# Performance work log

Measured on AMD Instinct MI355X. Metric: run time of the kernel, lower is better.

Reference implementation:

```python
import jax, jax.numpy as jnp
import numpy as np

DEPTH = 8
DIM = 512
D_INNER = 2 * DIM          # mamba expand=2
D_STATE = 16
D_CONV = 4
DT_RANK = DIM // 16        # 32
B, H, W = 2, 16, 16
EPS = 1e-5


def setup_inputs() -> dict:
    key = jax.random.key(0)
    ks = jax.random.split(key, 8)
    s = 0.02
    f32 = jnp.float32
    x = jax.random.normal(ks[0], (B, DIM, H, W), f32)
    in_proj_w = (jax.random.normal(ks[1], (DEPTH, 2 * D_INNER, DIM), f32) * s)
    conv_w = (jax.random.normal(ks[2], (DEPTH, D_INNER, D_CONV), f32) * 0.1)
    conv_b = jnp.zeros((DEPTH, D_INNER), f32)
    x_proj_w = (jax.random.normal(ks[3], (DEPTH, DT_RANK + 2 * D_STATE, D_INNER), f32) * s)
    dt_proj_w = (jax.random.normal(ks[4], (DEPTH, D_INNER, DT_RANK), f32) * s)
    dt_proj_b = (jax.random.normal(ks[5], (DEPTH, D_INNER), f32) * 0.1)
    # S4D-real init: A = -exp(A_log), A_log = log(1..d_state)
    A_log = jnp.log(jnp.broadcast_to(
        jnp.arange(1, D_STATE + 1, dtype=f32), (DEPTH, D_INNER, D_STATE)))
    D = jnp.ones((DEPTH, D_INNER), f32)
    out_proj_w = (jax.random.normal(ks[6], (DEPTH, DIM, D_INNER), f32) * s)
    norm_w = jnp.ones((DEPTH, DIM), f32)
    final_norm_w = jnp.ones((DIM,), f32)
    return {"x": x, "in_proj_w": in_proj_w, "conv_w": conv_w, "conv_b": conv_b,
            "x_proj_w": x_proj_w, "dt_proj_w": dt_proj_w, "dt_proj_b": dt_proj_b,
            "A_log": A_log, "D": D, "out_proj_w": out_proj_w,
            "norm_w": norm_w, "final_norm_w": final_norm_w}


def _rmsnorm(x, w):
    # rms_norm_ref: no mean subtraction, weight only (bias is None)
    return x * jax.lax.rsqrt(jnp.mean(x * x, axis=-1, keepdims=True) + EPS) * w


def _mixer(h, Wi, cw, cb, Wx, Wdt, bdt, A_log, Dv, Wo):
    # h: [B, L, DIM]
    xz = jnp.einsum('bld,ed->ble', h, Wi)            # [B,L,2*Di]
    xc, z = jnp.split(xz, 2, axis=-1)
    # causal depthwise conv1d (pad left d_conv-1), then SiLU
    xt = xc.transpose(0, 2, 1)                        # [B,Di,L]
    xt = jax.lax.conv_general_dilated(
        xt, cw[:, None, :], (1,), [(D_CONV - 1, 0)],
        feature_group_count=D_INNER)
    xc = jax.nn.silu((xt + cb[None, :, None]).transpose(0, 2, 1))  # [B,L,Di]
    dbl = jnp.einsum('bld,kd->blk', xc, Wx)           # [B,L,dt_rank+2N]
    dtr = dbl[..., :DT_RANK]
    Bm = dbl[..., DT_RANK:DT_RANK + D_STATE]          # [B,L,N]
    Cm = dbl[..., DT_RANK + D_STATE:]                 # [B,L,N]
    dt = jax.nn.softplus(jnp.einsum('blr,dr->bld', dtr, Wdt) + bdt)  # [B,L,Di]
    A = -jnp.exp(A_log)                               # [Di,N]
    dA = jnp.exp(dt[..., None] * A)                   # [B,L,Di,N]
    dBx = (dt * xc)[..., None] * Bm[:, :, None, :]    # [B,L,Di,N]

    def step(s, inp):
        a, bx, c = inp
        s = a * s + bx                                # [B,Di,N]
        return s, jnp.einsum('bdn,bn->bd', s, c)

    s0 = jnp.zeros((xc.shape[0], D_INNER, D_STATE), xc.dtype)
    _, ys = jax.lax.scan(step, s0, (dA.transpose(1, 0, 2, 3),
                                    dBx.transpose(1, 0, 2, 3),
                                    Cm.transpose(1, 0, 2)))
    y = ys.transpose(1, 0, 2) + Dv * xc               # [B,L,Di]
    y = y * jax.nn.silu(z)
    return jnp.einsum('bld,od->blo', y, Wo)           # [B,L,DIM]


def reference(x, in_proj_w, conv_w, conv_b, x_proj_w, dt_proj_w, dt_proj_b,
              A_log, D, out_proj_w, norm_w, final_norm_w):
    Bz, C, Hh, Ww = x.shape
    h = x.reshape(Bz, C, Hh * Ww).transpose(0, 2, 1)  # [B,L,C]
    residual = None
    for i in range(DEPTH):
        # fused add + RMSNorm (prenorm): residual <- h + residual; hn = norm(residual)
        residual = h if residual is None else h + residual
        hn = _rmsnorm(residual, norm_w[i])
        h = _mixer(hn, in_proj_w[i], conv_w[i], conv_b[i], x_proj_w[i],
                   dt_proj_w[i], dt_proj_b[i], A_log[i], D[i], out_proj_w[i])
    # Original module: with return_index=[depth-1], the returned tensor is the
    # post-loop `residual`; the final mixer output and final norm are dead code.
    out = residual.reshape(Bz, Hh, Ww, C)
    return out.transpose(0, 3, 1, 2)
```

## Files before the change

kernel.cpp:

```cpp
#include <hip/hip_runtime.h>
#include <hip/hip_bf16.h>

typedef __bf16 bf16x8 __attribute__((ext_vector_type(8)));
typedef float  f32x4  __attribute__((ext_vector_type(4)));

#define DIM    512
#define DINNER 1024
#define SEQL   256
#define NLAYER 7
#define LPAD   260
#define NCH    8
#define CLEN   32

#define N4WI (NLAYER * 2048 * 512 / 4)
#define N4WX (NLAYER * 64 * 1024 / 4)
#define N4WO (NLAYER * 512 * 1024 / 4)
#define N4ALL (N4WI + N4WX + N4WO)
#define NCASTB (N4ALL / 256)

__global__ __launch_bounds__(256) void k_castin(const float* __restrict__ Wi,
                                                const float* __restrict__ Wx,
                                                const float* __restrict__ Wo,
                                                const float* __restrict__ x,
                                                __hip_bfloat16* __restrict__ wib,
                                                __hip_bfloat16* __restrict__ wxb,
                                                __hip_bfloat16* __restrict__ wob,
                                                float* __restrict__ res,
                                                float* __restrict__ dblraw) {
  if (blockIdx.x >= NCASTB + 1024) {
    int i = (blockIdx.x - NCASTB - 1024) * 256 + threadIdx.x;
    reinterpret_cast<float4*>(dblraw)[i] = float4{0.f, 0.f, 0.f, 0.f};
    return;
  }
  if (blockIdx.x >= NCASTB) {
    int idx = (blockIdx.x - NCASTB) * 256 + threadIdx.x;
    int d = idx & (DIM - 1), l = (idx >> 9) & (SEQL - 1), b = idx >> 17;
    res[idx] = x[((size_t)((b << 9) + d) << 8) + l];
    return;
  }
  int i = blockIdx.x * 256 + threadIdx.x;
  const float* src; __hip_bfloat16* dst; int j;
  if (i < N4WI)             { src = Wi; dst = wib; j = i; }
  else if (i < N4WI + N4WX) { src = Wx; dst = wxb; j = i - N4WI; }
  else                      { src = Wo; dst = wob; j = i - N4WI - N4WX; }
  float4 v = reinterpret_cast<const float4*>(src)[j];
  struct alignas(8) B4 { __hip_bfloat16 a, b, c, d; };
  B4 o{ (__hip_bfloat16)v.x, (__hip_bfloat16)v.y, (__hip_bfloat16)v.z, (__hip_bfloat16)v.w };
  reinterpret_cast<B4*>(dst)[j] = o;
}

__global__ __launch_bounds__(1024) void k_front(const float* __restrict__ res,
                                                const float* __restrict__ nwL,
                                                const __hip_bfloat16* __restrict__ wiL,
                                                const __hip_bfloat16* __restrict__ wxL,
                                                const float4* __restrict__ cwL,
                                                const float* __restrict__ cbL,
                                                __hip_bfloat16* __restrict__ xcb,
                                                float* __restrict__ zT,
                                                float* __restrict__ dblraw) {
  __shared__ __align__(16) char smem[79872];
  __hip_bfloat16 (*s_hn)[520] = (__hip_bfloat16(*)[520])smem;
  float (*s_xz)[132] = (float(*)[132])(smem + 49920);
  __hip_bfloat16 (*s_xcb)[72] = (__hip_bfloat16(*)[72])(smem + 75264);
  const int tid = threadIdx.x, bid = blockIdx.x;
  const int wid = tid >> 6, lane = tid & 63;
  const int r = lane & 15, g = lane >> 4;
  const int ttile = bid >> 4, sl = bid & 15;
  const int t0 = ttile * 32, m0 = t0 - 3;
#pragma unroll
  for (int k = 0; k < 3; ++k) {
    int rw = wid * 3 + k;
    int grc = min(max(m0 + rw, 0), 511);
    const float* rr = res + ((size_t)grc << 9);
    float v[8]; float ssum = 0.f;
#pragma unroll
    for (int j2 = 0; j2 < 8; ++j2) { v[j2] = rr[lane + (j2 << 6)]; ssum = fmaf(v[j2], v[j2], ssum); }
#pragma unroll
    for (int m = 1; m < 64; m <<= 1) ssum += __shfl_xor(ssum, m);
    float inv = rsqrtf(ssum * (1.0f / 512.0f) + 1e-5f);
#pragma unroll
    for (int j2 = 0; j2 < 8; ++j2)
      s_hn[rw][lane + (j2 << 6)] = (__hip_bfloat16)(v[j2] * inv * nwL[lane + (j2 << 6)]);
  }
  __syncthreads();
  for (int j = wid; j < 24; j += 16) {
    int mf = j >> 3, cf = j & 7;
    int gcol = (cf < 4) ? (sl * 64 + cf * 16 + r) : (1024 + sl * 64 + (cf - 4) * 16 + r);
    const bf16x8* pb = reinterpret_cast<const bf16x8*>(wiL + (size_t)gcol * 512) + g;
    f32x4 acc = {0.f, 0.f, 0.f, 0.f};
#pragma unroll
    for (int kc = 0; kc < 16; ++kc) {
      bf16x8 a = *reinterpret_cast<const bf16x8*>(&s_hn[mf * 16 + r][kc * 32 + g * 8]);
      acc = __builtin_amdgcn_mfma_f32_16x16x32_bf16(a, pb[kc * 4], acc, 0, 0, 0);
    }
    int cc = (cf < 4) ? (cf * 16 + r) : (64 + (cf - 4) * 16 + r);
#pragma unroll
    for (int jj = 0; jj < 4; ++jj) s_xz[mf * 16 + g * 4 + jj][cc] = acc[jj];
  }
  __syncthreads();
  const int t0s = t0 & 255;
#pragma unroll
  for (int k = 0; k < 2; ++k) {
    int e = tid + (k << 10);
    int lloc = e >> 6, c = e & 63;
    int gd = sl * 64 + c;
    int lseq = t0s + lloc;
    float4 wv = cwL[gd];
    float accv = cbL[gd];
    accv = fmaf(s_xz[lloc + 3][c], wv.w, accv);
    if (lseq >= 1) accv = fmaf(s_xz[lloc + 2][c], wv.z, accv);
    if (lseq >= 2) accv = fmaf(s_xz[lloc + 1][c], wv.y, accv);
    if (lseq >= 3) accv = fmaf(s_xz[lloc + 0][c], wv.x, accv);
    float sv = accv / (1.f + __expf(-accv));
    __hip_bfloat16 hb = (__hip_bfloat16)sv;
    xcb[(size_t)(t0 + lloc) * 1024 + gd] = hb;
    s_xcb[lloc][c] = hb;
  }
  __syncthreads();
  if (wid < 8) {
    int mf = wid & 1, nf = wid >> 1;
    f32x4 acc = {0.f, 0.f, 0.f, 0.f};
#pragma unroll
    for (int kc = 0; kc < 2; ++kc) {
      bf16x8 a = *reinterpret_cast<const bf16x8*>(&s_xcb[mf * 16 + r][kc * 32 + g * 8]);
      bf16x8 bb = *reinterpret_cast<const bf16x8*>(
          wxL + (size_t)(nf * 16 + r) * 1024 + sl * 64 + kc * 32 + g * 8);
      acc = __builtin_amdgcn_mfma_f32_16x16x32_bf16(a, bb, acc, 0, 0, 0);
    }
#pragma unroll
    for (int jj = 0; jj < 4; ++jj)
      atomicAdd(&dblraw[(size_t)(t0 + mf * 16 + g * 4 + jj) * 64 + nf * 16 + r], acc[jj]);
  } else {
#pragma unroll
    for (int k = 0; k < 4; ++k) {
      int e = (tid - 512) + (k << 9);
      int lloc = e & 31, c = e >> 5;
      int gd = sl * 64 + c;
      zT[(size_t)gd * 512 + t0 + lloc] = s_xz[lloc + 3][64 + c];
    }
  }
}

__global__ __launch_bounds__(1024) void k_scan(const float* __restrict__ dblraw,
                                               const float* __restrict__ WdtL,
                                               const float* __restrict__ bdtL,
                                               const __hip_bfloat16* __restrict__ xcb,
                                               const float* __restrict__ zT,
                                               const float* __restrict__ alog,
                                               const float* __restrict__ dv,
                                               __hip_bfloat16* __restrict__ y) {
  __shared__ __align__(16) char smem[127744];
  float (*s_dt)[LPAD] = (float(*)[LPAD])(smem);
  float (*s_xc)[LPAD] = (float(*)[LPAD])(smem + 8320);
  float (*s_B)[LPAD]  = (float(*)[LPAD])(smem + 16640);
  float (*s_C)[LPAD]  = (float(*)[LPAD])(smem + 33280);
  float (*s_cp)[68]   = (float(*)[68]) (smem + 49920);
  float (*s_pe)[128]  = (float(*)[128])(smem + 119552);
  float (*s_se)[128]  = (float(*)[128])(smem + 123648);
  const int tid = threadIdx.x, bid = blockIdx.x;
  const int cg = tid >> 7;
  const int tt = tid & 127;
  const int n = tt & 15, dl = tt >> 4;
  const int b = bid >> 7;
  const int d0 = (bid & 127) << 3;
  const int d = d0 + dl;
  const int bL = b * SEQL;

#pragma unroll
  for (int k = 0; k < 2; ++k) {
    int fidx = tid + (k << 10);
    int l = fidx >> 3, q = fidx & 7;
    float4 v = *reinterpret_cast<const float4*>(dblraw + ((size_t)(bL + l) << 6) + 32 + (q << 2));
    float* dst = (q < 4) ? &s_B[(q & 3) << 2][l] : &s_C[(q & 3) << 2][l];
    dst[0] = v.x; dst[LPAD] = v.y; dst[2 * LPAD] = v.z; dst[3 * LPAD] = v.w;
  }
  if (tid < 256) {
    bf16x8 u = *reinterpret_cast<const bf16x8*>(xcb + (size_t)(bL + tid) * 1024 + d0);
#pragma unroll
    for (int e = 0; e < 8; ++e) s_xc[e][tid] = (float)u[e];
  }
  {
    int tk = tid >> 2;
    int cp = (tid & 3) << 1;
    const float* drow = dblraw + ((size_t)(bL + tk) << 6);
    float xv[32];
#pragma unroll
    for (int q = 0; q < 8; ++q) {
      float4 x4 = *reinterpret_cast<const float4*>(drow + (q << 2));
      xv[q * 4 + 0] = x4.x; xv[q * 4 + 1] = x4.y;
      xv[q * 4 + 2] = x4.z; xv[q * 4 + 3] = x4.w;
    }
#pragma unroll
    for (int kk = 0; kk < 2; ++kk) {
      int ch = cp + kk;
      const float4* wr = reinterpret_cast<const float4*>(WdtL + ((size_t)(d0 + ch) << 5));
      float acc = bdtL[d0 + ch];
#pragma unroll
      for (int q = 0; q < 8; ++q) {
        float4 w = wr[q];
        acc = fmaf(xv[q * 4 + 0], w.x, acc);
        acc = fmaf(xv[q * 4 + 1], w.y, acc);
        acc = fmaf(xv[q * 4 + 2], w.z, acc);
        acc = fmaf(xv[q * 4 + 3], w.w, acc);
      }
      s_dt[ch][tk] = (acc > 20.f) ? acc : log1pf(__expf(acc));
    }
  }
  __syncthreads();

  const float An = -__expf(alog[(size_t)d * 16 + n]);
  const int lb = cg << 5;

  float s = 0.f, P = 1.f;
#pragma unroll 2
  for (int l4 = 0; l4 < CLEN; l4 += 4) {
    const int l = lb + l4;
    float4 dt4 = *reinterpret_cast<const float4*>(&s_dt[dl][l]);
    float4 xc4 = *reinterpret_cast<const float4*>(&s_xc[dl][l]);
    float4 B4  = *reinterpret_cast<const float4*>(&s_B[n][l]);
    float dA;
    dA = __expf(dt4.x * An); P *= dA; s = fmaf(dA, s, dt4.x * xc4.x * B4.x);
    dA = __expf(dt4.y * An); P *= dA; s = fmaf(dA, s, dt4.y * xc4.y * B4.y);
    dA = __expf(dt4.z * An); P *= dA; s = fmaf(dA, s, dt4.z * xc4.z * B4.z);
    dA = __expf(dt4.w * An); P *= dA; s = fmaf(dA, s, dt4.w * xc4.w * B4.w);
  }
  s_pe[cg][tt] = P;
  s_se[cg][tt] = s;
  __syncthreads();

  float ss = 0.f;
  for (int c = 0; c < cg; ++c) ss = fmaf(s_pe[c][tt], ss, s_se[c][tt]);

  float s2 = ss;
#pragma unroll 2
  for (int l4 = 0; l4 < CLEN; l4 += 4) {
    const int l = lb + l4;
    float4 dt4 = *reinterpret_cast<const float4*>(&s_dt[dl][l]);
    float4 xc4 = *reinterpret_cast<const float4*>(&s_xc[dl][l]);
    float4 B4  = *reinterpret_cast<const float4*>(&s_B[n][l]);
    float4 C4  = *reinterpret_cast<const float4*>(&s_C[n][l]);
    float dA, c;
    dA = __expf(dt4.x * An); s2 = fmaf(dA, s2, dt4.x * xc4.x * B4.x); c = s2 * C4.x;
    c += __shfl_xor(c, 1); if (!(n & 1)) s_cp[l + 0][(dl << 3) | (n >> 1)] = c;
    dA = __expf(dt4.y * An); s2 = fmaf(dA, s2, dt4.y * xc4.y * B4.y); c = s2 * C4.y;
    c += __shfl_xor(c, 1); if (!(n & 1)) s_cp[l + 1][(dl << 3) | (n >> 1)] = c;
    dA = __expf(dt4.z * An); s2 = fmaf(dA, s2, dt4.z * xc4.z * B4.z); c = s2 * C4.z;
    c += __shfl_xor(c, 1); if (!(n & 1)) s_cp[l + 2][(dl << 3) | (n >> 1)] = c;
    dA = __expf(dt4.w * An); s2 = fmaf(dA, s2, dt4.w * xc4.w * B4.w); c = s2 * C4.w;
    c += __shfl_xor(c, 1); if (!(n & 1)) s_cp[l + 3][(dl << 3) | (n >> 1)] = c;
  }
  __syncthreads();

#pragma unroll
  for (int k = 0; k < 2; ++k) {
    int idx = tid + (k << 10);
    int l = idx >> 3, dd = idx & 7;
    const float* cr = &s_cp[l][dd << 3];
    float4 a0 = *reinterpret_cast<const float4*>(cr);
    float4 a1 = *reinterpret_cast<const float4*>(cr + 4);
    float sum = ((a0.x + a0.y) + (a0.z + a0.w)) + ((a1.x + a1.y) + (a1.z + a1.w));
    float xcv = s_xc[dd][l];
    float zv = zT[(size_t)(d0 + dd) * 512 + bL + l];
    float yv = (sum + dv[d0 + dd] * xcv) * (zv / (1.f + __expf(-zv)));
    y[((size_t)(bL + l) << 10) + d0 + dd] = (__hip_bfloat16)yv;
  }
}

template <bool FINAL>
__global__ __launch_bounds__(1024) void k_outproj(const __hip_bfloat16* __restrict__ y,
                                                  const __hip_bfloat16* __restrict__ woL,
                                                  float* __restrict__ res,
                                                  float* __restrict__ out,
                                                  float* __restrict__ dblraw) {
  __shared__ __align__(16) float s_red[16 * 1088 + 32 * 33];
  float (*s_tr)[33] = (float(*)[33])(s_red + 16 * 1088);
  const int tid = threadIdx.x, bid = blockIdx.x;
  const int wid = tid >> 6, lane = tid & 63;
  const int r = lane & 15, g = lane >> 4;
  int tile = bid >> 2, q = bid & 3;
  int row0 = (tile >> 3) * 64 + ((q >> 1) << 5);
  int col0 = (tile & 7) * 64 + ((q & 1) << 5);
  if (!FINAL && tid < 32)
    reinterpret_cast<float4*>(dblraw)[bid * 32 + tid] = float4{0.f, 0.f, 0.f, 0.f};
  {
    const bf16x8* pa0 = reinterpret_cast<const bf16x8*>(y + (size_t)(row0 + r) * 1024) + g + wid * 8;
    const bf16x8* pa1 = reinterpret_cast<const bf16x8*>(y + (size_t)(row0 + 16 + r) * 1024) + g + wid * 8;
    const bf16x8* pb0 = reinterpret_cast<const bf16x8*>(woL + (size_t)(col0 + r) * 1024) + g + wid * 8;
    const bf16x8* pb1 = reinterpret_cast<const bf16x8*>(woL + (size_t)(col0 + 16 + r) * 1024) + g + wid * 8;
    f32x4 zz = {0.f, 0.f, 0.f, 0.f};
    f32x4 acc[4] = {zz, zz, zz, zz};
#pragma unroll
    for (int kc = 0; kc < 2; ++kc) {
      bf16x8 a0 = pa0[kc * 4], a1 = pa1[kc * 4];
      bf16x8 b0 = pb0[kc * 4], b1 = pb1[kc * 4];
      acc[0] = __builtin_amdgcn_mfma_f32_16x16x32_bf16(a0, b0, acc[0], 0, 0, 0);
      acc[1] = __builtin_amdgcn_mfma_f32_16x16x32_bf16(a0, b1, acc[1], 0, 0, 0);
      acc[2] = __builtin_amdgcn_mfma_f32_16x16x32_bf16(a1, b0, acc[2], 0, 0, 0);
      acc[3] = __builtin_amdgcn_mfma_f32_16x16x32_bf16(a1, b1, acc[3], 0, 0, 0);
    }
    float* sr = s_red + wid * 1088;
#pragma unroll
    for (int e = 0; e < 4; ++e)
#pragma unroll
      for (int jj = 0; jj < 4; ++jj)
        sr[(((e >> 1) << 4) + (g << 2) + jj) * 34 + ((e & 1) << 4) + r] = acc[e][jj];
  }
  __syncthreads();
  {
    int rrow = tid >> 5, rcol = tid & 31;
    float sum = 0.f;
#pragma unroll
    for (int w = 0; w < 16; ++w) sum += s_red[w * 1088 + rrow * 34 + rcol];
    if (!FINAL) {
      res[(size_t)(row0 + rrow) * 512 + col0 + rcol] += sum;
    } else {
      s_tr[rcol][rrow] = res[(size_t)(row0 + rrow) * 512 + col0 + rcol] + sum;
    }
  }
  if (FINAL) {
    __syncthreads();
    int tl = tid & 31, tc = tid >> 5;
    int b = row0 >> 8, l0 = row0 & 255;
    out[(((size_t)((b << 9) + col0 + tc)) << 8) | (l0 + tl)] = s_tr[tc][tl];
  }
}

extern "C" void kernel_launch(void* const* d_in, const int* in_sizes, int n_in,
                              void* d_out, int out_size, void* d_ws, size_t ws_size,
                              hipStream_t stream) {
  (void)in_sizes; (void)n_in; (void)out_size; (void)ws_size;
  const float* x    = (const float*)d_in[0];
  const float* Wi   = (const float*)d_in[1];
  const float* cw   = (const float*)d_in[2];
  const float* cb   = (const float*)d_in[3];
  const float* Wx   = (const float*)d_in[4];
  const float* Wdt  = (const float*)d_in[5];
  const float* bdt  = (const float*)d_in[6];
  const float* Alog = (const float*)d_in[7];
  const float* Dv   = (const float*)d_in[8];
  const float* Wo   = (const float*)d_in[9];
  const float* nw   = (const float*)d_in[10];

  char* ws = (char*)d_ws;
  float*          res    = (float*)(ws + 0);
  __hip_bfloat16* xcb    = (__hip_bfloat16*)(ws + 1048576);
  float*          zT     = (float*)(ws + 4194304);
  float*          dblraw = (float*)(ws + 6291456);
  __hip_bfloat16* y      = (__hip_bfloat16*)(ws + 8454144);
  __hip_bfloat16* wib    = (__hip_bfloat16*)(ws + 10485760);
  __hip_bfloat16* wxb    = (__hip_bfloat16*)(ws + 25165824);
  __hip_bfloat16* wob    = (__hip_bfloat16*)(ws + 26083328);

  k_castin<<<NCASTB + 1024 + 32, 256, 0, stream>>>(Wi, Wx, Wo, x, wib, wxb, wob,
                                                   res, dblraw);

  for (int L = 0; L < NLAYER; ++L) {
    k_front<<<256, 1024, 0, stream>>>(res, nw + L * DIM,
                                      wib + (size_t)L * 2048 * 512,
                                      wxb + (size_t)L * 64 * 1024,
                                      (const float4*)cw + (size_t)L * DINNER,
                                      cb + L * DINNER, xcb, zT, dblraw);
    k_scan<<<256, 1024, 0, stream>>>(dblraw,
                                     Wdt + (size_t)L * DINNER * 32, bdt + L * DINNER,
                                     xcb, zT,
                                     Alog + (size_t)L * DINNER * 16, Dv + L * DINNER, y);
    if (L < NLAYER - 1)
      k_outproj<false><<<256, 1024, 0, stream>>>(y, wob + (size_t)L * 512 * 1024, res,
                                                 nullptr, dblraw);
    else
      k_outproj<true><<<256, 1024, 0, stream>>>(y, wob + (size_t)L * 512 * 1024, res,
                                                (float*)d_out, dblraw);
  }
}
```

Measured before the change: 306.5 us.

## Split scan into smaller blocks and reduce state outputs fully via shuffles

The selective-scan kernel now uses 512 blocks of 512 threads, each covering 4 inner channels instead of 8, which cuts shared memory per block from about 125KB to about 49KB. This lets more blocks run per CU and fills the GPU with more independent work. The C-weighted state sum is now reduced across all 16 state lanes with a shuffle tree and written once per channel, replacing the partial shared-memory buffer and its 8-way reduction pass. In exchange, the dt/B/C loads from dblraw are repeated across twice as many blocks, and each thread buffers 16 values in registers.

```diff
diff --git a/kernel.cpp b/kernel.cpp
--- a/kernel.cpp
+++ b/kernel.cpp
@@ -2,6 +2,7 @@
 #include <hip/hip_bf16.h>
 
 typedef __bf16 bf16x8 __attribute__((ext_vector_type(8)));
+typedef __bf16 bf16x4 __attribute__((ext_vector_type(4)));
 typedef float  f32x4  __attribute__((ext_vector_type(4)));
 
 #define DIM    512
@@ -141,47 +142,47 @@
   }
 }
 
-__global__ __launch_bounds__(1024) void k_scan(const float* __restrict__ dblraw,
-                                               const float* __restrict__ WdtL,
-                                               const float* __restrict__ bdtL,
-                                               const __hip_bfloat16* __restrict__ xcb,
-                                               const float* __restrict__ zT,
-                                               const float* __restrict__ alog,
-                                               const float* __restrict__ dv,
-                                               __hip_bfloat16* __restrict__ y) {
-  __shared__ __align__(16) char smem[127744];
+__global__ __launch_bounds__(512) void k_scan(const float* __restrict__ dblraw,
+                                              const float* __restrict__ WdtL,
+                                              const float* __restrict__ bdtL,
+                                              const __hip_bfloat16* __restrict__ xcb,
+                                              const float* __restrict__ zT,
+                                              const float* __restrict__ alog,
+                                              const float* __restrict__ dv,
+                                              __hip_bfloat16* __restrict__ y) {
+  __shared__ __align__(16) char smem[49792];
   float (*s_dt)[LPAD] = (float(*)[LPAD])(smem);
-  float (*s_xc)[LPAD] = (float(*)[LPAD])(smem + 8320);
-  float (*s_B)[LPAD]  = (float(*)[LPAD])(smem + 16640);
-  float (*s_C)[LPAD]  = (float(*)[LPAD])(smem + 33280);
-  float (*s_cp)[68]   = (float(*)[68]) (smem + 49920);
-  float (*s_pe)[128]  = (float(*)[128])(smem + 119552);
-  float (*s_se)[128]  = (float(*)[128])(smem + 123648);
+  float (*s_xc)[LPAD] = (float(*)[LPAD])(smem + 4160);
+  float (*s_B)[LPAD]  = (float(*)[LPAD])(smem + 8320);
+  float (*s_C)[LPAD]  = (float(*)[LPAD])(smem + 24960);
+  float (*s_pe)[64]   = (float(*)[64]) (smem + 41600);
+  float (*s_se)[64]   = (float(*)[64]) (smem + 43648);
+  float (*s_ys)[4]    = (float(*)[4])  (smem + 45696);
   const int tid = threadIdx.x, bid = blockIdx.x;
-  const int cg = tid >> 7;
-  const int tt = tid & 127;
+  const int cg = tid >> 6;
+  const int tt = tid & 63;
   const int n = tt & 15, dl = tt >> 4;
-  const int b = bid >> 7;
-  const int d0 = (bid & 127) << 3;
+  const int b = bid >> 8;
+  const int d0 = (bid & 255) << 2;
   const int d = d0 + dl;
   const int bL = b * SEQL;
 
 #pragma unroll
-  for (int k = 0; k < 2; ++k) {
-    int fidx = tid + (k << 10);
+  for (int k = 0; k < 4; ++k) {
+    int fidx = tid + (k << 9);
     int l = fidx >> 3, q = fidx & 7;
     float4 v = *reinterpret_cast<const float4*>(dblraw + ((size_t)(bL + l) << 6) + 32 + (q << 2));
     float* dst = (q < 4) ? &s_B[(q & 3) << 2][l] : &s_C[(q & 3) << 2][l];
     dst[0] = v.x; dst[LPAD] = v.y; dst[2 * LPAD] = v.z; dst[3 * LPAD] = v.w;
   }
   if (tid < 256) {
-    bf16x8 u = *reinterpret_cast<const bf16x8*>(xcb + (size_t)(bL + tid) * 1024 + d0);
-#pragma unroll
-    for (int e = 0; e < 8; ++e) s_xc[e][tid] = (float)u[e];
+    bf16x4 u = *reinterpret_cast<const bf16x4*>(xcb + (size_t)(bL + tid) * 1024 + d0);
+#pragma unroll
+    for (int e = 0; e < 4; ++e) s_xc[e][tid] = (float)u[e];
   }
   {
-    int tk = tid >> 2;
-    int cp = (tid & 3) << 1;
+    int tk = tid >> 1;
+    int cp = (tid & 1) << 1;
     const float* drow = dblraw + ((size_t)(bL + tk) << 6);
     float xv[32];
 #pragma unroll
@@ -232,33 +233,44 @@
   for (int c = 0; c < cg; ++c) ss = fmaf(s_pe[c][tt], ss, s_se[c][tt]);
 
   float s2 = ss;
-#pragma unroll 2
-  for (int l4 = 0; l4 < CLEN; l4 += 4) {
-    const int l = lb + l4;
-    float4 dt4 = *reinterpret_cast<const float4*>(&s_dt[dl][l]);
-    float4 xc4 = *reinterpret_cast<const float4*>(&s_xc[dl][l]);
-    float4 B4  = *reinterpret_cast<const float4*>(&s_B[n][l]);
-    float4 C4  = *reinterpret_cast<const float4*>(&s_C[n][l]);
-    float dA, c;
-    dA = __expf(dt4.x * An); s2 = fmaf(dA, s2, dt4.x * xc4.x * B4.x); c = s2 * C4.x;
-    c += __shfl_xor(c, 1); if (!(n & 1)) s_cp[l + 0][(dl << 3) | (n >> 1)] = c;
-    dA = __expf(dt4.y * An); s2 = fmaf(dA, s2, dt4.y * xc4.y * B4.y); c = s2 * C4.y;
-    c += __shfl_xor(c, 1); if (!(n & 1)) s_cp[l + 1][(dl << 3) | (n >> 1)] = c;
-    dA = __expf(dt4.z * An); s2 = fmaf(dA, s2, dt4.z * xc4.z * B4.z); c = s2 * C4.z;
-    c += __shfl_xor(c, 1); if (!(n & 1)) s_cp[l + 2][(dl << 3) | (n >> 1)] = c;
-    dA = __expf(dt4.w * An); s2 = fmaf(dA, s2, dt4.w * xc4.w * B4.w); c = s2 * C4.w;
-    c += __shfl_xor(c, 1); if (!(n & 1)) s_cp[l + 3][(dl << 3) | (n >> 1)] = c;
+#pragma unroll
+  for (int half = 0; half < 2; ++half) {
+    const int base = lb + (half << 4);
+    float cr[16];
+#pragma unroll
+    for (int l4 = 0; l4 < 16; l4 += 4) {
+      const int l = base + l4;
+      float4 dt4 = *reinterpret_cast<const float4*>(&s_dt[dl][l]);
+      float4 xc4 = *reinterpret_cast<const float4*>(&s_xc[dl][l]);
+      float4 B4  = *reinterpret_cast<const float4*>(&s_B[n][l]);
+      float4 C4  = *reinterpret_cast<const float4*>(&s_C[n][l]);
+      float dA;
+      dA = __expf(dt4.x * An); s2 = fmaf(dA, s2, dt4.x * xc4.x * B4.x); cr[l4 + 0] = s2 * C4.x;
+      dA = __expf(dt4.y * An); s2 = fmaf(dA, s2, dt4.y * xc4.y * B4.y); cr[l4 + 1] = s2 * C4.y;
+      dA = __expf(dt4.z * An); s2 = fmaf(dA, s2, dt4.z * xc4.z * B4.z); cr[l4 + 2] = s2 * C4.z;
+      dA = __expf(dt4.w * An); s2 = fmaf(dA, s2, dt4.w * xc4.w * B4.w); cr[l4 + 3] = s2 * C4.w;
+    }
+#pragma unroll
+    for (int i = 0; i < 16; ++i) {
+      float c = cr[i];
+      c += __shfl_xor(c, 1);
+      c += __shfl_xor(c, 2);
+      c += __shfl_xor(c, 4);
+      c += __shfl_xor(c, 8);
+      cr[i] = c;
+    }
+    if (n == 0) {
+#pragma unroll
+      for (int i = 0; i < 16; ++i) s_ys[base + i][dl] = cr[i];
+    }
   }
   __syncthreads();
 
 #pragma unroll
   for (int k = 0; k < 2; ++k) {
-    int idx = tid + (k << 10);
-    int l = idx >> 3, dd = idx & 7;
-    const float* cr = &s_cp[l][dd << 3];
-    float4 a0 = *reinterpret_cast<const float4*>(cr);
-    float4 a1 = *reinterpret_cast<const float4*>(cr + 4);
-    float sum = ((a0.x + a0.y) + (a0.z + a0.w)) + ((a1.x + a1.y) + (a1.z + a1.w));
+    int idx = tid + (k << 9);
+    int l = idx >> 2, dd = idx & 3;
+    float sum = s_ys[l][dd];
     float xcv = s_xc[dd][l];
     float zv = zT[(size_t)(d0 + dd) * 512 + bL + l];
     float yv = (sum + dv[d0 + dd] * xcv) * (zv / (1.f + __expf(-zv)));
@@ -360,10 +372,10 @@
                                       wxb + (size_t)L * 64 * 1024,
                                       (const float4*)cw + (size_t)L * DINNER,
                                       cb + L * DINNER, xcb, zT, dblraw);
-    k_scan<<<256, 1024, 0, stream>>>(dblraw,
-                                     Wdt + (size_t)L * DINNER * 32, bdt + L * DINNER,
-                                     xcb, zT,
-                                     Alog + (size_t)L * DINNER * 16, Dv + L * DINNER, y);
+    k_scan<<<512, 512, 0, stream>>>(dblraw,
+                                    Wdt + (size_t)L * DINNER * 32, bdt + L * DINNER,
+                                    xcb, zT,
+                                    Alog + (size_t)L * DINNER * 16, Dv + L * DINNER, y);
     if (L < NLAYER - 1)
       k_outproj<false><<<256, 1024, 0, stream>>>(y, wob + (size_t)L * 512 * 1024, res,
                                                  nullptr, dblraw);
```

New measurement: 302.5 us, median of 2. Within noise of the previous version (-1.3%).
